# Kernel optimization log

Hardware: AMD Instinct MI355X
Metric: run time of the kernel (lower is better)

The kernel has to match this reference:

```python
import jax, jax.numpy as jnp
import numpy as np

HIDDEN = 1024
HEADS = 16
HEAD_DIM = HIDDEN // HEADS
BATCH = 1
SEQ = 4096
SCALE = 1.0 / np.sqrt(HEAD_DIM)


def setup_inputs() -> dict:
    key = jax.random.key(0)
    ks = jax.random.split(key, 5)
    s = 0.02
    return {
        "hidden_states": jax.random.normal(ks[0], (BATCH, SEQ, HIDDEN), jnp.float32),
        "qkv_w": jax.random.normal(ks[1], (3 * HIDDEN, HIDDEN), jnp.float32) * s,
        "qkv_b": jax.random.normal(ks[2], (3 * HIDDEN,), jnp.float32) * s,
        "out_w": jax.random.normal(ks[3], (HIDDEN, HIDDEN), jnp.float32) * s,
        "out_b": jax.random.normal(ks[4], (HIDDEN,), jnp.float32) * s,
    }


def reference(hidden_states, qkv_w, qkv_b, out_w, out_b):
    B, S, H = hidden_states.shape
    # fused QKV projection (torch Linear: x @ W^T + b)
    qkv = hidden_states @ qkv_w.T + qkv_b              # [B, S, 3H]
    qkv = qkv.reshape(B, S, 3, HEADS, HEAD_DIM)
    qkv = jnp.transpose(qkv, (2, 0, 3, 1, 4))          # [3, B, nh, S, hd]
    q, k, v = qkv[0] * SCALE, qkv[1], qkv[2]
    # ring attention over all KV chunks == full softmax attention
    scores = jnp.einsum('bhqd,bhkd->bhqk', q, k)       # [B, nh, S, S]
    probs = jax.nn.softmax(scores, axis=-1)
    ctx = jnp.einsum('bhqk,bhkd->bhqd', probs, v)      # [B, nh, S, hd]
    ctx = jnp.transpose(ctx, (0, 2, 1, 3)).reshape(B, S, H)
    return ctx @ out_w.T + out_b
```

## Files before the change

kernel.cpp:

```cpp
#include <hip/hip_runtime.h>

#define SEQ 4096
#define HID 1024
#define NHEADS 16
#define HDIM 64
#define QK_SCALE 0.1803368801111204f

typedef float  f32x4 __attribute__((ext_vector_type(4)));
typedef int    i32x4 __attribute__((ext_vector_type(4)));
typedef int    i32x2 __attribute__((ext_vector_type(2)));
typedef __bf16 bf16x8 __attribute__((ext_vector_type(8)));
typedef unsigned short u16;
typedef unsigned int   u32;

static __device__ __forceinline__ u16 f2bf(float f) {
  u32 u = __builtin_bit_cast(u32, f);
  return (u16)((u + 0x7FFFu + ((u >> 16) & 1u)) >> 16);
}
static __device__ __forceinline__ int cvtpk(float lo, float hi) {
  int r;
  asm("v_cvt_pk_bf16_f32 %0, %1, %2" : "=v"(r) : "v"(lo), "v"(hi));
  return r;
}
static __device__ __forceinline__ f32x4 exp2v(f32x4 x) {
  f32x4 o;
  o.x = __builtin_amdgcn_exp2f(x.x);
  o.y = __builtin_amdgcn_exp2f(x.y);
  o.z = __builtin_amdgcn_exp2f(x.z);
  o.w = __builtin_amdgcn_exp2f(x.w);
  return o;
}
static __device__ __forceinline__ float sum4(f32x4 x) {
  return (x.x + x.y) + (x.z + x.w);
}
static __device__ __forceinline__ f32x4 mfma16(i32x4 a, i32x4 b, f32x4 c) {
  return __builtin_amdgcn_mfma_f32_16x16x32_bf16(
      __builtin_bit_cast(bf16x8, a), __builtin_bit_cast(bf16x8, b), c, 0, 0, 0);
}

#define GLD(gsrc, lds_dst)                                        \
  __builtin_amdgcn_global_load_lds(                               \
      (const __attribute__((address_space(1))) void*)(gsrc),      \
      (__attribute__((address_space(3))) void*)(lds_dst), 16, 0, 0)

__global__ __launch_bounds__(256) void cvt_kernel(
    const float* __restrict__ X, const float* __restrict__ Wq,
    const float* __restrict__ Wo, u16* __restrict__ Xb,
    u16* __restrict__ Wqb, u16* __restrict__ Wob) {
  const int u = blockIdx.x * 256 + threadIdx.x;
  const float* src; u16* dst; int local;
  if (u < 524288)       { src = X;  dst = Xb;  local = u; }
  else if (u < 917504)  { src = Wq; dst = Wqb; local = u - 524288; }
  else                  { src = Wo; dst = Wob; local = u - 917504; }
  const int row = local >> 7, gu = local & 127;
  const int w = gu & 7, blk = gu >> 3;
  const int ks = w >> 2, q2 = w & 3;
  const float* s = src + (size_t)row * 1024 + blk * 64 + ks * 32 + q2 * 4;
  float4 x0 = *(const float4*)s;
  float4 x1 = *(const float4*)(s + 16);
  i32x4 o = {cvtpk(x0.x, x0.y), cvtpk(x0.z, x0.w),
             cvtpk(x1.x, x1.y), cvtpk(x1.z, x1.w)};
  *(i32x4*)(dst + (size_t)row * 1024 + blk * 64 + w * 8) = o;
}

static __device__ __forceinline__ void gemm_tile(
    const u16* __restrict__ A, const u16* __restrict__ B,
    int mb, int nb, u16 (*LA)[128][64], u16 (*LB)[128][64],
    f32x4 acc[4][4]) {
  const int t = threadIdx.x, lane = t & 63, wv = t >> 6;
  const int g = lane >> 4, r = lane & 15;
  const int wr = wv >> 1, wc = wv & 1;
  const int lr = lane >> 3, sl = lane & 7;

  const u16* pa = A + (size_t)(mb + wv * 32 + lr) * 1024 + ((sl ^ lr) << 3);
  const u16* pb = B + (size_t)(nb + wv * 32 + lr) * 1024 + ((sl ^ lr) << 3);

  const u16* afp[4][2];
  const u16* bfp[4][2];
#pragma unroll
  for (int i = 0; i < 4; ++i)
#pragma unroll
    for (int ks = 0; ks < 2; ++ks) {
      const int sw = r & 7;
      afp[i][ks] = &LA[0][wr * 64 + i * 16 + r][(((ks * 4 + g) ^ sw) << 3)];
      bfp[i][ks] = &LB[0][wc * 64 + i * 16 + r][(((ks * 4 + g) ^ sw) << 3)];
    }
#pragma unroll
  for (int i = 0; i < 4; ++i)
#pragma unroll
    for (int j = 0; j < 4; ++j) acc[i][j] = (f32x4)0.0f;

#pragma unroll
  for (int j = 0; j < 4; ++j) {
    GLD(pa + j * 8 * 1024, &LA[0][wv * 32 + j * 8][0]);
    GLD(pb + j * 8 * 1024, &LB[0][wv * 32 + j * 8][0]);
  }
  pa += 64; pb += 64;
  __syncthreads();

#define GEMM_STEP(BU, PRE)                                                  \
  {                                                                         \
    if (PRE) {                                                              \
      _Pragma("unroll")                                                     \
      for (int j = 0; j < 4; ++j) {                                         \
        GLD(pa + j * 8 * 1024, &LA[(BU) ^ 1][wv * 32 + j * 8][0]);          \
        GLD(pb + j * 8 * 1024, &LB[(BU) ^ 1][wv * 32 + j * 8][0]);          \
      }                                                                     \
      pa += 64; pb += 64;                                                   \
    }                                                                       \
    i32x4 af[4][2], bf[4][2];                                               \
    _Pragma("unroll")                                                       \
    for (int i = 0; i < 4; ++i)                                             \
      _Pragma("unroll")                                                     \
      for (int ks = 0; ks < 2; ++ks) {                                      \
        af[i][ks] = *(const i32x4*)(afp[i][ks] + (BU) * 8192);              \
        bf[i][ks] = *(const i32x4*)(bfp[i][ks] + (BU) * 8192);              \
      }                                                                     \
    __builtin_amdgcn_s_setprio(1);                                          \
    _Pragma("unroll")                                                       \
    for (int ks = 0; ks < 2; ++ks)                                          \
      _Pragma("unroll")                                                     \
      for (int i = 0; i < 4; ++i)                                           \
        _Pragma("unroll")                                                   \
        for (int j = 0; j < 4; ++j)                                         \
          acc[i][j] = mfma16(af[i][ks], bf[j][ks], acc[i][j]);              \
    __builtin_amdgcn_s_setprio(0);                                          \
    __syncthreads();                                                        \
  }

  for (int kk = 0; kk < 8; ++kk) {
    GEMM_STEP(0, true)
    GEMM_STEP(1, (kk < 7))
  }
#undef GEMM_STEP
}

__global__ __launch_bounds__(256) void qkv_kernel(
    const u16* __restrict__ A, const u16* __restrict__ Bw,
    const float* __restrict__ BI, u16* __restrict__ qws,
    u16* __restrict__ kws, u16* __restrict__ vws) {
  __shared__ u16 LA[2][128][64];
  __shared__ u16 LB[2][128][64];
  const int t = threadIdx.x, lane = t & 63, wv = t >> 6;
  const int g = lane >> 4, r = lane & 15;
  const int wr = wv >> 1, wc = wv & 1;
  const int mb = blockIdx.x * 128, nb = blockIdx.y * 128;

  f32x4 acc[4][4];
  gemm_tile(A, Bw, mb, nb, LA, LB, acc);

#pragma unroll
  for (int ni = 0; ni < 4; ni++) {
    const int n = nb + wc * 64 + ni * 16 + r;
    const float bias = BI[n];
    const int which = n >> 10;
    const int h = (n >> 6) & 15;
    const int d = n & 63;
    u16* dst = (which == 0) ? qws : (which == 1) ? kws : vws;
    const float sc = (which == 0) ? QK_SCALE : 1.0f;
    const int dq = (which == 2)
        ? d
        : ((d & 32) | (((d >> 2) & 3) << 3) | (((d >> 4) & 1) << 2) | (d & 3));
#pragma unroll
    for (int mi = 0; mi < 4; mi++) {
      const int m0 = mb + wr * 64 + mi * 16 + g * 4;
#pragma unroll
      for (int e = 0; e < 4; e += 2) {
        float v0 = (acc[mi][ni][e] + bias) * sc;
        float v1 = (acc[mi][ni][e + 1] + bias) * sc;
        int w = cvtpk(v0, v1);
        dst[((size_t)h * SEQ + m0 + e) * HDIM + dq] = (u16)w;
        dst[((size_t)h * SEQ + m0 + e + 1) * HDIM + dq] = (u16)(w >> 16);
      }
    }
  }
}

__global__ __launch_bounds__(256, 4) void attn_kernel(
    const u16* __restrict__ qws, const u16* __restrict__ kws,
    const u16* __restrict__ vws, u16* __restrict__ ctx) {
  __shared__ u16 Kl[2][64][64];
  __shared__ u16 Vl[2][16][256];
  const int t = threadIdx.x;
  const int lane = t & 63, wv = t >> 6;
  const int g = lane >> 4, r = lane & 15;

  const int fb = blockIdx.x;
  const int swz = (fb & 7) * 128 + (fb >> 3);
  const int h = swz >> 6;
  const int qb = (swz & 63) * 64 + wv * 16;

  i32x4 qf[2];
#pragma unroll
  for (int db = 0; db < 2; db++)
    qf[db] = *(const i32x4*)(qws +
        ((size_t)(h * SEQ + qb + r) * HDIM + db * 32 + g * 8));

  f32x4 acc[4];
  f32x4 l4 = (f32x4)0.0f;
  const f32x4 zero4 = (f32x4)0.0f;
#pragma unroll
  for (int dc = 0; dc < 4; dc++) acc[dc] = (f32x4)0.0f;

  const u16* kh_base = kws + (size_t)h * SEQ * HDIM;
  const u16* vh_base = vws + (size_t)h * SEQ * HDIM;

  const u16* kgA = kh_base + (size_t)(16 * wv + (lane >> 3)) * HDIM +
                   (((lane & 7) ^ ((lane >> 3) & 7)) << 3);
  const u16* kgB = kgA + 8 * HDIM;
  const u16* vgA = vh_base +
                   (size_t)(wv * 16 + ((lane & 31) >> 1)) * HDIM +
                   (((((lane >> 5) << 1) | (lane & 1))) << 3);
  const u16* vgB = vgA + 32;

  const u16* kfp0[4];
  const u16* kfp1[4];
#pragma unroll
  for (int kt = 0; kt < 4; ++kt) {
    const int R = kt * 16 + r;
    const int sw = R & 7;
    kfp0[kt] = &Kl[0][R][(g ^ sw) << 3];
    kfp1[kt] = &Kl[0][R][((4 + g) ^ sw) << 3];
  }
  const u32 vbase = (u32)(size_t)(&Vl[0][0][0]) + (u32)lane * 8;

  GLD(kgA, &Kl[0][wv * 16][0]);
  GLD(kgB, &Kl[0][wv * 16 + 8][0]);
  GLD(vgA, &Vl[0][wv * 4][0]);
  GLD(vgB, &Vl[0][wv * 4 + 2][0]);
  kgA += 4096; kgB += 4096; vgA += 4096; vgB += 4096;
  __syncthreads();

#define ATTN_STEP(B, PRE)                                                   \
  {                                                                         \
    if (PRE) {                                                              \
      GLD(kgA, &Kl[(B) ^ 1][wv * 16][0]);                                   \
      GLD(kgB, &Kl[(B) ^ 1][wv * 16 + 8][0]);                               \
      GLD(vgA, &Vl[(B) ^ 1][wv * 4][0]);                                    \
      GLD(vgB, &Vl[(B) ^ 1][wv * 4 + 2][0]);                                \
      kgA += 4096; kgB += 4096; vgA += 4096; vgB += 4096;                   \
    }                                                                       \
    f32x4 st[4];                                                            \
    __builtin_amdgcn_s_setprio(1);                                          \
    _Pragma("unroll")                                                       \
    for (int kt = 0; kt < 4; ++kt) {                                        \
      i32x4 kf0 = *(const i32x4*)(kfp0[kt] + (B) * 4096);                   \
      i32x4 kf1 = *(const i32x4*)(kfp1[kt] + (B) * 4096);                   \
      st[kt] = mfma16(kf0, qf[0], zero4);                                   \
      st[kt] = mfma16(kf1, qf[1], st[kt]);                                  \
    }                                                                       \
    __builtin_amdgcn_s_setprio(0);                                          \
                                         \
    f32x4 p0 = exp2v(st[0]);                                                \
    f32x4 p1 = exp2v(st[1]);                                                \
    f32x4 p2 = exp2v(st[2]);                                                \
    f32x4 p3 = exp2v(st[3]);                                                \
    l4 += p0; l4 += p1; l4 += p2; l4 += p3;                                 \
    i32x4 pf0 = {cvtpk(p0.x, p0.y), cvtpk(p0.z, p0.w),                      \
                 cvtpk(p1.x, p1.y), cvtpk(p1.z, p1.w)};                     \
    i32x4 pf1 = {cvtpk(p2.x, p2.y), cvtpk(p2.z, p2.w),                      \
                 cvtpk(p3.x, p3.y), cvtpk(p3.z, p3.w)};                     \
    const u32 vb = vbase + (B) * 8192;                                      \
    __builtin_amdgcn_s_setprio(1);                                          \
    _Pragma("unroll")                                                       \
    for (int dc = 0; dc < 4; ++dc) {                                        \
      i32x2 t0, t1, t2, t3;                                                 \
      asm volatile(                                                         \
          "ds_read_b64_tr_b16 %0, %4 offset:0\n\t"                          \
          "ds_read_b64_tr_b16 %1, %4 offset:2048\n\t"                       \
          "ds_read_b64_tr_b16 %2, %4 offset:4096\n\t"                       \
          "ds_read_b64_tr_b16 %3, %4 offset:6144"                           \
          : "=&v"(t0), "=&v"(t1), "=&v"(t2), "=&v"(t3)                      \
          : "v"(vb + dc * 512));                                            \
      asm volatile("s_waitcnt lgkmcnt(0)" ::: "memory");                    \
      __builtin_amdgcn_sched_barrier(0);                                    \
      i32x4 vf0 = {t0.x, t0.y, t1.x, t1.y};                                 \
      i32x4 vf1 = {t2.x, t2.y, t3.x, t3.y};                                 \
      acc[dc] = mfma16(pf0, vf0, acc[dc]);                                  \
      acc[dc] = mfma16(pf1, vf1, acc[dc]);                                  \
    }                                                                       \
    __builtin_amdgcn_s_setprio(0);                                          \
    __syncthreads();                                                        \
  }

  for (int cc = 0; cc < 32; ++cc) {
    ATTN_STEP(0, true)
    ATTN_STEP(1, (cc < 31))
  }
#undef ATTN_STEP

  float lsum = sum4(l4);
  lsum += __shfl_xor(lsum, 16);
  lsum += __shfl_xor(lsum, 32);

#pragma unroll
  for (int rr = 0; rr < 4; ++rr) {
    const float lr_ = __shfl(lsum, 4 * g + rr);
    const float inv = 1.0f / lr_;
    const int s_ = qb + 4 * g + rr;
#pragma unroll
    for (int dc = 0; dc < 4; ++dc) {
      const int shuf = ((dc >> 1) << 5) | ((r >> 2) << 3) | ((dc & 1) << 2) | (r & 3);
      ctx[(size_t)s_ * HID + h * HDIM + shuf] = f2bf(acc[dc][rr] * inv);
    }
  }
}

__global__ __launch_bounds__(256) void out_kernel(
    const u16* __restrict__ A, const u16* __restrict__ Bw,
    const float* __restrict__ BI, float* __restrict__ out) {
  __shared__ u16 LA[2][128][64];
  __shared__ u16 LB[2][128][64];
  const int t = threadIdx.x, lane = t & 63, wv = t >> 6;
  const int g = lane >> 4, r = lane & 15;
  const int wr = wv >> 1, wc = wv & 1;
  const int mb = blockIdx.x * 128, nb = blockIdx.y * 128;

  f32x4 acc[4][4];
  gemm_tile(A, Bw, mb, nb, LA, LB, acc);

#pragma unroll
  for (int ni = 0; ni < 4; ni++) {
    const int n = nb + wc * 64 + ni * 16 + r;
    const float bias = BI[n];
#pragma unroll
    for (int mi = 0; mi < 4; mi++) {
      const int m0 = mb + wr * 64 + mi * 16 + g * 4;
#pragma unroll
      for (int e = 0; e < 4; e++)
        out[(size_t)(m0 + e) * HID + n] = acc[mi][ni][e] + bias;
    }
  }
}

extern "C" void kernel_launch(void* const* d_in, const int* in_sizes, int n_in,
                              void* d_out, int out_size, void* d_ws, size_t ws_size,
                              hipStream_t stream) {
  const float* X    = (const float*)d_in[0];
  const float* Wqkv = (const float*)d_in[1];
  const float* Bqkv = (const float*)d_in[2];
  const float* Wout = (const float*)d_in[3];
  const float* Bout = (const float*)d_in[4];
  float* out = (float*)d_out;

  const size_t per = (size_t)NHEADS * SEQ * HDIM;
  u16* qws = (u16*)d_ws;
  u16* kws = qws + per;
  u16* vws = kws + per;
  u16* xbctx = vws + per;
  u16* wqb = xbctx + per;
  u16* wob = wqb + (size_t)3072 * 1024;

  cvt_kernel<<<4096, 256, 0, stream>>>(X, Wqkv, Wout, xbctx, wqb, wob);
  qkv_kernel<<<dim3(32, 24), 256, 0, stream>>>(xbctx, wqb, Bqkv, qws, kws, vws);
  attn_kernel<<<dim3(1024), 256, 0, stream>>>(qws, kws, vws, xbctx);
  out_kernel<<<dim3(32, 8), 256, 0, stream>>>(xbctx, wob, Bout, out);
}
```

Before: 146.8 us.

## Process two query tiles per wave in attention to reuse K/V fragments

Each wave now handles 32 query rows (two 16-row tiles) instead of 16, so every K fragment and transposed V read from shared memory feeds two MFMAs. Blocks cover 128 queries, the grid is halved to 512 blocks, and the launch bound drops to 2 waves per EU to allow the extra registers. The aim is to halve K/V global-to-LDS traffic and LDS reads per query. The cost is more registers and fewer resident blocks, with 512 blocks over the MI355X's CUs possibly giving poorer occupancy and tail balance.

```diff
diff --git a/kernel.cpp b/kernel.cpp
--- a/kernel.cpp
+++ b/kernel.cpp
@@ -176,7 +176,7 @@
   }
 }
 
-__global__ __launch_bounds__(256, 4) void attn_kernel(
+__global__ __launch_bounds__(256, 2) void attn_kernel(
     const u16* __restrict__ qws, const u16* __restrict__ kws,
     const u16* __restrict__ vws, u16* __restrict__ ctx) {
   __shared__ u16 Kl[2][64][64];
@@ -186,21 +186,27 @@
   const int g = lane >> 4, r = lane & 15;
 
   const int fb = blockIdx.x;
-  const int swz = (fb & 7) * 128 + (fb >> 3);
-  const int h = swz >> 6;
-  const int qb = (swz & 63) * 64 + wv * 16;
-
-  i32x4 qf[2];
-#pragma unroll
-  for (int db = 0; db < 2; db++)
-    qf[db] = *(const i32x4*)(qws +
-        ((size_t)(h * SEQ + qb + r) * HDIM + db * 32 + g * 8));
-
-  f32x4 acc[4];
-  f32x4 l4 = (f32x4)0.0f;
+  const int swz = (fb & 7) * 64 + (fb >> 3);
+  const int h = swz >> 5;
+  const int qb = (swz & 31) * 128 + wv * 32;
+
+  i32x4 qf[2][2];
+#pragma unroll
+  for (int qt = 0; qt < 2; qt++)
+#pragma unroll
+    for (int db = 0; db < 2; db++)
+      qf[qt][db] = *(const i32x4*)(qws +
+          ((size_t)(h * SEQ + qb + qt * 16 + r) * HDIM + db * 32 + g * 8));
+
+  f32x4 acc[2][4];
+  f32x4 l4[2];
   const f32x4 zero4 = (f32x4)0.0f;
 #pragma unroll
-  for (int dc = 0; dc < 4; dc++) acc[dc] = (f32x4)0.0f;
+  for (int qt = 0; qt < 2; qt++) {
+    l4[qt] = (f32x4)0.0f;
+#pragma unroll
+    for (int dc = 0; dc < 4; dc++) acc[qt][dc] = (f32x4)0.0f;
+  }
 
   const u16* kh_base = kws + (size_t)h * SEQ * HDIM;
   const u16* vh_base = vws + (size_t)h * SEQ * HDIM;
@@ -240,26 +246,32 @@
       GLD(vgB, &Vl[(B) ^ 1][wv * 4 + 2][0]);                                \
       kgA += 4096; kgB += 4096; vgA += 4096; vgB += 4096;                   \
     }                                                                       \
-    f32x4 st[4];                                                            \
+    f32x4 st[2][4];                                                         \
     __builtin_amdgcn_s_setprio(1);                                          \
     _Pragma("unroll")                                                       \
     for (int kt = 0; kt < 4; ++kt) {                                        \
       i32x4 kf0 = *(const i32x4*)(kfp0[kt] + (B) * 4096);                   \
       i32x4 kf1 = *(const i32x4*)(kfp1[kt] + (B) * 4096);                   \
-      st[kt] = mfma16(kf0, qf[0], zero4);                                   \
-      st[kt] = mfma16(kf1, qf[1], st[kt]);                                  \
+      st[0][kt] = mfma16(kf0, qf[0][0], zero4);                             \
+      st[0][kt] = mfma16(kf1, qf[0][1], st[0][kt]);                         \
+      st[1][kt] = mfma16(kf0, qf[1][0], zero4);                             \
+      st[1][kt] = mfma16(kf1, qf[1][1], st[1][kt]);                         \
     }                                                                       \
     __builtin_amdgcn_s_setprio(0);                                          \
-                                         \
-    f32x4 p0 = exp2v(st[0]);                                                \
-    f32x4 p1 = exp2v(st[1]);                                                \
-    f32x4 p2 = exp2v(st[2]);                                                \
-    f32x4 p3 = exp2v(st[3]);                                                \
-    l4 += p0; l4 += p1; l4 += p2; l4 += p3;                                 \
-    i32x4 pf0 = {cvtpk(p0.x, p0.y), cvtpk(p0.z, p0.w),                      \
-                 cvtpk(p1.x, p1.y), cvtpk(p1.z, p1.w)};                     \
-    i32x4 pf1 = {cvtpk(p2.x, p2.y), cvtpk(p2.z, p2.w),                      \
-                 cvtpk(p3.x, p3.y), cvtpk(p3.z, p3.w)};                     \
+                          \
+    i32x4 pf[2][2];                                                         \
+    _Pragma("unroll")                                                       \
+    for (int qt = 0; qt < 2; ++qt) {                                        \
+      f32x4 p0 = exp2v(st[qt][0]);                                          \
+      f32x4 p1 = exp2v(st[qt][1]);                                          \
+      f32x4 p2 = exp2v(st[qt][2]);                                          \
+      f32x4 p3 = exp2v(st[qt][3]);                                          \
+      l4[qt] += p0; l4[qt] += p1; l4[qt] += p2; l4[qt] += p3;               \
+      pf[qt][0] = (i32x4){cvtpk(p0.x, p0.y), cvtpk(p0.z, p0.w),             \
+                          cvtpk(p1.x, p1.y), cvtpk(p1.z, p1.w)};            \
+      pf[qt][1] = (i32x4){cvtpk(p2.x, p2.y), cvtpk(p2.z, p2.w),             \
+                          cvtpk(p3.x, p3.y), cvtpk(p3.z, p3.w)};            \
+    }                                                                       \
     const u32 vb = vbase + (B) * 8192;                                      \
     __builtin_amdgcn_s_setprio(1);                                          \
     _Pragma("unroll")                                                       \
@@ -276,8 +288,10 @@
       __builtin_amdgcn_sched_barrier(0);                                    \
       i32x4 vf0 = {t0.x, t0.y, t1.x, t1.y};                                 \
       i32x4 vf1 = {t2.x, t2.y, t3.x, t3.y};                                 \
-      acc[dc] = mfma16(pf0, vf0, acc[dc]);                                  \
-      acc[dc] = mfma16(pf1, vf1, acc[dc]);                                  \
+      acc[0][dc] = mfma16(pf[0][0], vf0, acc[0][dc]);                       \
+      acc[0][dc] = mfma16(pf[0][1], vf1, acc[0][dc]);                       \
+      acc[1][dc] = mfma16(pf[1][0], vf0, acc[1][dc]);                       \
+      acc[1][dc] = mfma16(pf[1][1], vf1, acc[1][dc]);                       \
     }                                                                       \
     __builtin_amdgcn_s_setprio(0);                                          \
     __syncthreads();                                                        \
@@ -289,19 +303,21 @@
   }
 #undef ATTN_STEP
 
-  float lsum = sum4(l4);
-  lsum += __shfl_xor(lsum, 16);
-  lsum += __shfl_xor(lsum, 32);
-
-#pragma unroll
-  for (int rr = 0; rr < 4; ++rr) {
-    const float lr_ = __shfl(lsum, 4 * g + rr);
-    const float inv = 1.0f / lr_;
-    const int s_ = qb + 4 * g + rr;
-#pragma unroll
-    for (int dc = 0; dc < 4; ++dc) {
-      const int shuf = ((dc >> 1) << 5) | ((r >> 2) << 3) | ((dc & 1) << 2) | (r & 3);
-      ctx[(size_t)s_ * HID + h * HDIM + shuf] = f2bf(acc[dc][rr] * inv);
+#pragma unroll
+  for (int qt = 0; qt < 2; ++qt) {
+    float lsum = sum4(l4[qt]);
+    lsum += __shfl_xor(lsum, 16);
+    lsum += __shfl_xor(lsum, 32);
+#pragma unroll
+    for (int rr = 0; rr < 4; ++rr) {
+      const float lr_ = __shfl(lsum, 4 * g + rr);
+      const float inv = 1.0f / lr_;
+      const int s_ = qb + qt * 16 + 4 * g + rr;
+#pragma unroll
+      for (int dc = 0; dc < 4; ++dc) {
+        const int shuf = ((dc >> 1) << 5) | ((r >> 2) << 3) | ((dc & 1) << 2) | (r & 3);
+        ctx[(size_t)s_ * HID + h * HDIM + shuf] = f2bf(acc[qt][dc][rr] * inv);
+      }
     }
   }
 }
@@ -353,6 +369,6 @@
 
   cvt_kernel<<<4096, 256, 0, stream>>>(X, Wqkv, Wout, xbctx, wqb, wob);
   qkv_kernel<<<dim3(32, 24), 256, 0, stream>>>(xbctx, wqb, Bqkv, qws, kws, vws);
-  attn_kernel<<<dim3(1024), 256, 0, stream>>>(qws, kws, vws, xbctx);
+  attn_kernel<<<dim3(512), 256, 0, stream>>>(qws, kws, vws, xbctx);
   out_kernel<<<dim3(32, 8), 256, 0, stream>>>(xbctx, wob, Bout, out);
 }
```

Result: faster. 141.0 us (-4.0%).
